# Kernel optimization log

Measured on AMD Instinct MI355X. Metric: run time of the kernel, lower is better.

The kernel has to match this reference:

```python
import jax, jax.numpy as jnp
import numpy as np

LN_EPS = 1e-5


def setup_inputs() -> dict:
    key = jax.random.key(0)
    ks = jax.random.split(key, 8)
    B, S, D = 8, 2048, 1024
    H, A, DA = 16, 4, 64
    sd = 1.0 / np.sqrt(D)
    inp = {
        "x": jax.random.normal(ks[0], (B, S, D), jnp.float32),
        "Wq": jax.random.normal(ks[1], (D, H * DA), jnp.float32) * sd,
        "bq": jnp.zeros((H * DA,), jnp.float32),
        "Wk": jax.random.normal(ks[2], (D, H * DA), jnp.float32) * sd,
        "bk": jnp.zeros((H * DA,), jnp.float32),
        "Wv": jax.random.normal(ks[3], (D, H * DA), jnp.float32) * sd,
        "bv": jnp.zeros((H * DA,), jnp.float32),
        "Wr": jax.random.normal(ks[4], (D, H), jnp.float32) * sd,
        "br": jnp.zeros((H,), jnp.float32),
        "gamma": jnp.ones((H,), jnp.float32),
        "beta": jnp.zeros((H,), jnp.float32),
        "Wo": jax.random.normal(ks[5], (A * DA, D), jnp.float32) * (1.0 / np.sqrt(A * DA)),
        "bo": jnp.zeros((D,), jnp.float32),
        "n_active": 4,
    }
    return inp


def reference(x, Wq, bq, Wk, bk, Wv, bv, Wr, br, gamma, beta, Wo, bo, n_active):
    B, S, D = x.shape
    H = Wr.shape[1]
    DA = Wq.shape[1] // H
    A = int(n_active)

    # --- router (route_type == 'mean', noise == 0) ---
    r = jnp.mean(x @ Wr + br, axis=1)                      # [B, H]
    mu = jnp.mean(r, axis=-1, keepdims=True)
    var = jnp.mean((r - mu) ** 2, axis=-1, keepdims=True)
    rn = (r - mu) * jax.lax.rsqrt(var + LN_EPS) * gamma + beta
    dist = jax.nn.softmax(rn, axis=1)                      # [B, H]

    # top-k heads; boolean-mask gather in torch selects in ascending head order
    _, idx = jax.lax.top_k(dist, A)                        # [B, A]
    idx_sorted = jnp.sort(idx, axis=-1)                    # [B, A]
    dist_dense = jnp.take_along_axis(dist, idx_sorted, axis=-1)  # [B, A]

    def proj(W, b):
        # [B, S, H*DA] -> [B, H, S, DA]
        return (x @ W + b).reshape(B, S, H, DA).transpose(0, 2, 1, 3)

    gidx = idx_sorted[:, :, None, None]                    # [B, A, 1, 1]
    Q = jnp.take_along_axis(proj(Wq, bq), gidx, axis=1)    # [B, A, S, DA]
    K = jnp.take_along_axis(proj(Wk, bk), gidx, axis=1)
    V = jnp.take_along_axis(proj(Wv, bv), gidx, axis=1)

    scale = 1.0 / jnp.sqrt(jnp.asarray(DA, x.dtype))
    scores = jnp.einsum("basd,batd->bast", Q, K) * scale   # [B, A, S, S]
    attn = jax.nn.softmax(scores, axis=-1)
    O = jnp.einsum("bast,batd->basd", attn, V)             # [B, A, S, DA]

    O = dist_dense[:, :, None, None] * O                   # gated combine
    O_final = O.transpose(0, 2, 1, 3).reshape(B, S, A * DA)
    Z = O_final @ Wo + bo                                  # [B, S, D]
    return Z
```

## Files before the change

kernel.cpp:

```cpp
#include <hip/hip_runtime.h>
#include <math.h>

#define B_ 8
#define S_ 2048
#define D_ 1024
#define H_ 16
#define A_ 4
#define DA_ 64
#define LN_EPS 1e-5f
#define QSCALE 0.1803368801111204f
#define MREF 20.0f

typedef __bf16 bf16x8 __attribute__((ext_vector_type(8)));
typedef __bf16 bf16x4 __attribute__((ext_vector_type(4)));
typedef float f32x4 __attribute__((ext_vector_type(4)));
typedef unsigned short u16x8 __attribute__((ext_vector_type(8)));
typedef unsigned short u16x4 __attribute__((ext_vector_type(4)));

static const size_t OFF_PARTIAL = 0;
static const size_t OFF_IDX     = (size_t)1 << 20;
static const size_t OFF_DIST    = ((size_t)1 << 20) + 1024;
static const size_t OFF_WOT     = ((size_t)1 << 20) + ((size_t)1 << 19);
static const size_t OFF_XB      = (size_t)2 << 20;
static const size_t OFF_OFIN    = OFF_XB;
static const size_t OFF_WT      = (size_t)34 << 20;
static const size_t OFF_Q       = (size_t)40 << 20;
static const size_t OFF_K       = (size_t)48 << 20;
static const size_t OFF_V       = (size_t)56 << 20;

__global__ __launch_bounds__(256) void k_partial(const float* __restrict__ x,
                                                 float* __restrict__ partial,
                                                 __bf16* __restrict__ xb) {
  const int c = blockIdx.x, b = blockIdx.y, t = threadIdx.x;
  const size_t base = ((size_t)b * S_ + (size_t)c * 64) * D_;
  f32x4 acc = {0.f, 0.f, 0.f, 0.f};
  for (int s = 0; s < 64; ++s) {
    f32x4 v = *(const f32x4*)(x + base + (size_t)s * D_ + 4 * t);
    acc += v;
    bf16x4 o;
    #pragma unroll
    for (int j = 0; j < 4; ++j) o[j] = (__bf16)v[j];
    *(bf16x4*)(xb + base + (size_t)s * D_ + 4 * t) = o;
  }
  *(f32x4*)(partial + ((size_t)b * 32 + c) * D_ + 4 * t) = acc;
}

__global__ __launch_bounds__(256) void k_wt(const float* __restrict__ Wq,
                                            const float* __restrict__ Wk,
                                            const float* __restrict__ Wv,
                                            __bf16* __restrict__ Wt) {
  __shared__ float tsh[64][65];
  const int n0 = blockIdx.x * 64, k0 = blockIdx.y * 64, z = blockIdx.z;
  const float* W = (z == 0) ? Wq : (z == 1) ? Wk : Wv;
  const int t = threadIdx.x;
  #pragma unroll
  for (int i = 0; i < 4; ++i) {
    int r = i * 16 + (t >> 4), c = (t & 15) * 4;
    f32x4 v = *(const f32x4*)(W + (size_t)(k0 + r) * (H_ * DA_) + n0 + c);
    tsh[r][c + 0] = v[0]; tsh[r][c + 1] = v[1]; tsh[r][c + 2] = v[2]; tsh[r][c + 3] = v[3];
  }
  __syncthreads();
  #pragma unroll
  for (int i = 0; i < 4; ++i) {
    int n = i * 16 + (t >> 4), kc = (t & 15) * 4;
    bf16x4 o;
    #pragma unroll
    for (int j = 0; j < 4; ++j) o[j] = (__bf16)tsh[kc + j][n];
    *(bf16x4*)(Wt + (size_t)z * 1048576 + (size_t)(n0 + n) * 1024 + k0 + kc) = o;
  }
}

__global__ __launch_bounds__(256) void k_wto(const float* __restrict__ Wo,
                                             __bf16* __restrict__ WoT) {
  __shared__ float tsh[64][65];
  const int n0 = blockIdx.x * 64, k0 = blockIdx.y * 64;
  const int t = threadIdx.x;
  #pragma unroll
  for (int i = 0; i < 4; ++i) {
    int r = i * 16 + (t >> 4), c = (t & 15) * 4;
    f32x4 v = *(const f32x4*)(Wo + (size_t)(k0 + r) * D_ + n0 + c);
    tsh[r][c + 0] = v[0]; tsh[r][c + 1] = v[1]; tsh[r][c + 2] = v[2]; tsh[r][c + 3] = v[3];
  }
  __syncthreads();
  #pragma unroll
  for (int i = 0; i < 4; ++i) {
    int n = i * 16 + (t >> 4), kc = (t & 15) * 4;
    bf16x4 o;
    #pragma unroll
    for (int j = 0; j < 4; ++j) o[j] = (__bf16)tsh[kc + j][n];
    *(bf16x4*)(WoT + (size_t)(n0 + n) * (A_ * DA_) + k0 + kc) = o;
  }
}

__global__ __launch_bounds__(256) void k_stats(const float* __restrict__ partial,
                                               const float* __restrict__ Wr,
                                               const float* __restrict__ br,
                                               const float* __restrict__ gamma,
                                               const float* __restrict__ beta,
                                               int* __restrict__ idx_out,
                                               float* __restrict__ dist_out) {
  __shared__ float xbar[D_];
  __shared__ float rsh[H_];
  const int b = blockIdx.x, t = threadIdx.x;
  #pragma unroll
  for (int j = 0; j < 4; ++j) {
    int d = j * 256 + t;
    float s = 0.f;
    for (int c = 0; c < 32; ++c) s += partial[((size_t)b * 32 + c) * D_ + d];
    xbar[d] = s * (1.0f / S_);
  }
  __syncthreads();
  const int w = t >> 6, lane = t & 63;
  #pragma unroll
  for (int i = 0; i < 4; ++i) {
    int h = w * 4 + i;
    float s = 0.f;
    #pragma unroll
    for (int j = 0; j < 16; ++j) {
      int d = j * 64 + lane;
      s += xbar[d] * Wr[d * H_ + h];
    }
    for (int off = 32; off; off >>= 1) s += __shfl_down(s, off);
    if (lane == 0) rsh[h] = s + br[h];
  }
  __syncthreads();
  if (t == 0) {
    float r[H_];
    float mu = 0.f;
    for (int h = 0; h < H_; ++h) { r[h] = rsh[h]; mu += r[h]; }
    mu *= (1.0f / H_);
    float var = 0.f;
    for (int h = 0; h < H_; ++h) { float d = r[h] - mu; var += d * d; }
    var *= (1.0f / H_);
    float inv = rsqrtf(var + LN_EPS);
    float rn[H_], ex[H_];
    float mx = -1e30f;
    for (int h = 0; h < H_; ++h) {
      rn[h] = (r[h] - mu) * inv * gamma[h] + beta[h];
      mx = fmaxf(mx, rn[h]);
    }
    float sum = 0.f;
    for (int h = 0; h < H_; ++h) { ex[h] = expf(rn[h] - mx); sum += ex[h]; }
    int sel[A_];
    bool used[H_] = {false};
    for (int a = 0; a < A_; ++a) {
      int best = 0; float bv = -1.f;
      for (int h = 0; h < H_; ++h)
        if (!used[h] && ex[h] > bv) { bv = ex[h]; best = h; }
      used[best] = true; sel[a] = best;
    }
    for (int i = 0; i < A_; ++i)
      for (int j = i + 1; j < A_; ++j)
        if (sel[j] < sel[i]) { int tmp = sel[i]; sel[i] = sel[j]; sel[j] = tmp; }
    float invsum = 1.0f / sum;
    for (int a = 0; a < A_; ++a) {
      idx_out[b * A_ + a] = sel[a];
      dist_out[b * A_ + a] = ex[sel[a]] * invsum;
    }
  }
}

__global__ __launch_bounds__(256) void k_qkv_mfma(const __bf16* __restrict__ xb,
                                                  const __bf16* __restrict__ Wt,
                                                  const float* __restrict__ bq,
                                                  const float* __restrict__ bk,
                                                  const float* __restrict__ bv,
                                                  const int* __restrict__ idx,
                                                  __bf16* __restrict__ Q,
                                                  __bf16* __restrict__ K,
                                                  __bf16* __restrict__ Vt_g) {
  __shared__ unsigned short As[64][72];
  __shared__ unsigned short Bs[192][72];
  const int qt = blockIdx.x, ba = blockIdx.y;
  const int b = ba >> 2;
  const int head64 = idx[ba] * 64;
  const int t = threadIdx.x;
  const int w = t >> 6, l = t & 63, x = l & 15, g = l >> 4;
  const int MO = (w >> 1) * 32, NO = (w & 1) * 96;

  const unsigned short* xbu = (const unsigned short*)xb;
  const unsigned short* Wtu = (const unsigned short*)Wt;
  const size_t xbase = ((size_t)b * S_ + (size_t)qt * 64) * D_;

  u16x8 areg[2], breg[6];
  #pragma unroll
  for (int i = 0; i < 2; ++i) {
    int id = t + 256 * i, row = id >> 3, ch = id & 7;
    areg[i] = *(const u16x8*)(xbu + xbase + (size_t)row * D_ + ch * 8);
  }
  #pragma unroll
  for (int i = 0; i < 6; ++i) {
    int id = t + 256 * i, row = id >> 3, ch = id & 7;
    int m = row >> 6, nn = row & 63;
    breg[i] = *(const u16x8*)(Wtu + (size_t)m * 1048576 +
                              (size_t)(head64 + nn) * 1024 + ch * 8);
  }

  f32x4 acc[2][6];
  #pragma unroll
  for (int mf = 0; mf < 2; ++mf)
    #pragma unroll
    for (int nf = 0; nf < 6; ++nf) acc[mf][nf] = (f32x4){0.f, 0.f, 0.f, 0.f};

  for (int k0 = 0; k0 < D_; k0 += 64) {
    __syncthreads();
    #pragma unroll
    for (int i = 0; i < 2; ++i) {
      int id = t + 256 * i, row = id >> 3, ch = id & 7;
      *(u16x8*)&As[row][ch * 8] = areg[i];
    }
    #pragma unroll
    for (int i = 0; i < 6; ++i) {
      int id = t + 256 * i, row = id >> 3, ch = id & 7;
      *(u16x8*)&Bs[row][ch * 8] = breg[i];
    }
    __syncthreads();
    {
      int kn = (k0 + 64 < D_) ? k0 + 64 : k0;
      #pragma unroll
      for (int i = 0; i < 2; ++i) {
        int id = t + 256 * i, row = id >> 3, ch = id & 7;
        areg[i] = *(const u16x8*)(xbu + xbase + (size_t)row * D_ + kn + ch * 8);
      }
      #pragma unroll
      for (int i = 0; i < 6; ++i) {
        int id = t + 256 * i, row = id >> 3, ch = id & 7;
        int m = row >> 6, nn = row & 63;
        breg[i] = *(const u16x8*)(Wtu + (size_t)m * 1048576 +
                                  (size_t)(head64 + nn) * 1024 + kn + ch * 8);
      }
    }
    #pragma unroll
    for (int ks = 0; ks < 2; ++ks) {
      bf16x8 af[2], bfr[6];
      #pragma unroll
      for (int mf = 0; mf < 2; ++mf)
        af[mf] = *(const bf16x8*)&As[MO + mf * 16 + x][ks * 32 + g * 8];
      #pragma unroll
      for (int nf = 0; nf < 6; ++nf)
        bfr[nf] = *(const bf16x8*)&Bs[NO + nf * 16 + x][ks * 32 + g * 8];
      #pragma unroll
      for (int mf = 0; mf < 2; ++mf)
        #pragma unroll
        for (int nf = 0; nf < 6; ++nf)
          acc[mf][nf] = __builtin_amdgcn_mfma_f32_16x16x32_bf16(af[mf], bfr[nf], acc[mf][nf], 0, 0, 0);
    }
  }

  #pragma unroll
  for (int nf = 0; nf < 6; ++nf) {
    const int n = NO + nf * 16;
    const int m = n >> 6;
    if (m == 2) continue;
    const float* bias = (m == 0) ? bq : bk;
    __bf16* out = (m == 0) ? Q : K;
    const float sc = (m == 0) ? QSCALE : 1.0f;
    const int nn = (n & 63) + x;
    const float bval = bias[head64 + nn];
    #pragma unroll
    for (int mf = 0; mf < 2; ++mf)
      #pragma unroll
      for (int r = 0; r < 4; ++r) {
        int srow = qt * 64 + MO + mf * 16 + 4 * g + r;
        float val = (acc[mf][nf][r] + bval) * sc;
        out[((size_t)ba * S_ + srow) * DA_ + nn] = (__bf16)val;
      }
  }

  __syncthreads();
  if (w & 1) {
    #pragma unroll
    for (int nf = 2; nf < 6; ++nf) {
      const int da = (nf - 2) * 16 + x;
      const float bval = bv[head64 + da];
      #pragma unroll
      for (int mf = 0; mf < 2; ++mf)
        #pragma unroll
        for (int r = 0; r < 4; ++r) {
          int ls = MO + mf * 16 + 4 * g + r;
          __bf16 vb = (__bf16)(acc[mf][nf][r] + bval);
          As[da][ls] = __builtin_bit_cast(unsigned short, vb);
        }
    }
  }
  __syncthreads();
  {
    unsigned short* Vtu = (unsigned short*)Vt_g;
    const int vrow = t >> 3, vch = t & 7;
    u16x8 v0 = *(const u16x8*)&As[vrow][vch * 8];
    u16x8 v1 = *(const u16x8*)&As[vrow + 32][vch * 8];
    const size_t vb0 = (size_t)ba * DA_ * S_;
    *(u16x8*)(Vtu + vb0 + (size_t)vrow * S_ + qt * 64 + vch * 8) = v0;
    *(u16x8*)(Vtu + vb0 + (size_t)(vrow + 32) * S_ + qt * 64 + vch * 8) = v1;
  }
}

__global__ __launch_bounds__(256, 4) void k_attn_mfma(const __bf16* __restrict__ Qg,
                                                      const __bf16* __restrict__ Kg,
                                                      const __bf16* __restrict__ Vtg,
                                                      const float* __restrict__ dist,
                                                      __bf16* __restrict__ Ofin) {
  __shared__ unsigned short QPs[64 * 72];
  __shared__ unsigned short Ks[64 * 64];
  __shared__ unsigned short Vt[64 * 64];

  const int qt = blockIdx.x, ba = blockIdx.y;
  const int b = ba >> 2, a = ba & 3;
  const int t = threadIdx.x;
  const int w = t >> 6, l = t & 63, x = l & 15, g = l >> 4;

  const unsigned short* Qgu = (const unsigned short*)Qg;
  const unsigned short* Kgu = (const unsigned short*)Kg;
  const unsigned short* Vgu = (const unsigned short*)Vtg;

  const size_t kvbase = (size_t)ba * S_ * DA_;
  const size_t vbase  = (size_t)ba * DA_ * S_;

  const int krow = t >> 3, kch = t & 7;

  u16x8 kreg0, kreg1, vreg0, vreg1;
  kreg0 = *(const u16x8*)(Kgu + kvbase + (size_t)(krow) * 64 + kch * 8);
  kreg1 = *(const u16x8*)(Kgu + kvbase + (size_t)(krow + 32) * 64 + kch * 8);
  vreg0 = *(const u16x8*)(Vgu + vbase + (size_t)krow * S_ + kch * 8);
  vreg1 = *(const u16x8*)(Vgu + vbase + (size_t)(krow + 32) * S_ + kch * 8);

  {
    const size_t qbase = ((size_t)ba * S_ + (size_t)qt * 64) * DA_;
    #pragma unroll
    for (int i = 0; i < 2; ++i) {
      int row = (t >> 3) + 32 * i;
      int ch = t & 7;
      u16x8 v = *(const u16x8*)(Qgu + qbase + (size_t)row * 64 + ch * 8);
      *(u16x8*)&QPs[row * 64 + ((ch ^ (row & 7)) << 3)] = v;
    }
  }
  __syncthreads();

  bf16x8 qf[2];
  #pragma unroll
  for (int ks = 0; ks < 2; ++ks) {
    int row = w * 16 + x;
    int ch = (g + 4 * ks) ^ (row & 7);
    qf[ks] = *(const bf16x8*)&QPs[row * 64 + (ch << 3)];
  }

  f32x4 o_[4];
  float l_lane = 0.f;
  #pragma unroll
  for (int nf = 0; nf < 4; ++nf) o_[nf] = (f32x4){0.f, 0.f, 0.f, 0.f};

  for (int kt = 0; kt < 32; ++kt) {
    __syncthreads();
    *(u16x8*)&Ks[krow * 64 + ((kch ^ (krow & 7)) << 3)] = kreg0;
    *(u16x8*)&Vt[krow * 64 + ((kch ^ (krow & 7)) << 3)] = vreg0;
    {
      int row1 = krow + 32;
      *(u16x8*)&Ks[row1 * 64 + ((kch ^ (row1 & 7)) << 3)] = kreg1;
      *(u16x8*)&Vt[row1 * 64 + ((kch ^ (row1 & 7)) << 3)] = vreg1;
    }
    __syncthreads();

    {
      int ktn = (kt + 1 < 32) ? kt + 1 : kt;
      kreg0 = *(const u16x8*)(Kgu + kvbase + (size_t)(ktn * 64 + krow) * 64 + kch * 8);
      kreg1 = *(const u16x8*)(Kgu + kvbase + (size_t)(ktn * 64 + krow + 32) * 64 + kch * 8);
      vreg0 = *(const u16x8*)(Vgu + vbase + (size_t)krow * S_ + ktn * 64 + kch * 8);
      vreg1 = *(const u16x8*)(Vgu + vbase + (size_t)(krow + 32) * S_ + ktn * 64 + kch * 8);
    }

    f32x4 s_[4];
    #pragma unroll
    for (int nf = 0; nf < 4; ++nf) s_[nf] = (f32x4){-MREF, -MREF, -MREF, -MREF};
    #pragma unroll
    for (int ks = 0; ks < 2; ++ks) {
      bf16x8 kf[4];
      #pragma unroll
      for (int nf = 0; nf < 4; ++nf) {
        int kvrow = nf * 16 + x;
        int ch = (g + 4 * ks) ^ (kvrow & 7);
        kf[nf] = *(const bf16x8*)&Ks[kvrow * 64 + (ch << 3)];
      }
      #pragma unroll
      for (int nf = 0; nf < 4; ++nf)
        s_[nf] = __builtin_amdgcn_mfma_f32_16x16x32_bf16(kf[nf], qf[ks], s_[nf], 0, 0, 0);
    }

    float rs = 0.f;
    #pragma unroll
    for (int nf = 0; nf < 4; ++nf)
      #pragma unroll
      for (int r = 0; r < 4; ++r) {
        float p = exp2f(s_[nf][r]);
        s_[nf][r] = p;
        rs += p;
      }
    l_lane += rs;

    #pragma unroll
    for (int nf = 0; nf < 4; ++nf) {
      u16x4 pk;
      #pragma unroll
      for (int r = 0; r < 4; ++r) {
        __bf16 pb = (__bf16)s_[nf][r];
        pk[r] = __builtin_bit_cast(unsigned short, pb);
      }
      *(u16x4*)&QPs[(w * 16 + x) * 72 + nf * 16 + 4 * g] = pk;
    }

    #pragma unroll
    for (int ks = 0; ks < 2; ++ks) {
      bf16x8 pf = *(const bf16x8*)&QPs[(w * 16 + x) * 72 + (g * 8 + ks * 32)];
      bf16x8 vf[4];
      #pragma unroll
      for (int nf = 0; nf < 4; ++nf) {
        int darow = nf * 16 + x;
        int ch = (g + 4 * ks) ^ (darow & 7);
        vf[nf] = *(const bf16x8*)&Vt[darow * 64 + (ch << 3)];
      }
      #pragma unroll
      for (int nf = 0; nf < 4; ++nf)
        o_[nf] = __builtin_amdgcn_mfma_f32_16x16x32_bf16(pf, vf[nf], o_[nf], 0, 0, 0);
    }
  }

  const float dd = dist[ba];
  {
    float lf = l_lane;
    lf += __shfl_xor(lf, 16);
    lf += __shfl_xor(lf, 32);
    float inv[4];
    #pragma unroll
    for (int r = 0; r < 4; ++r) {
      float lr = __shfl(lf, 4 * g + r);
      inv[r] = dd / lr;
    }
    #pragma unroll
    for (int nf = 0; nf < 4; ++nf)
      #pragma unroll
      for (int r = 0; r < 4; ++r) {
        int row = qt * 64 + w * 16 + 4 * g + r;
        int col = nf * 16 + x;
        Ofin[((size_t)b * S_ + row) * (A_ * DA_) + a * DA_ + col] =
            (__bf16)(o_[nf][r] * inv[r]);
      }
  }
}

__global__ __launch_bounds__(256) void k_oproj_mfma(const __bf16* __restrict__ Of,
                                                    const __bf16* __restrict__ WoT,
                                                    const float* __restrict__ bo,
                                                    float* __restrict__ Z) {
  __shared__ unsigned short As[128][72];
  __shared__ unsigned short Bs[128][72];
  const int nt = blockIdx.x, mt = blockIdx.y;
  const int t = threadIdx.x;
  const int w = t >> 6, l = t & 63, x = l & 15, g = l >> 4;
  const int MO = (w >> 1) * 64, NO = (w & 1) * 64;

  const unsigned short* Ofu = (const unsigned short*)Of;
  const unsigned short* Wu  = (const unsigned short*)WoT;

  u16x8 areg[4], breg[4];
  #pragma unroll
  for (int i = 0; i < 4; ++i) {
    int id = t + 256 * i, row = id >> 3, ch = id & 7;
    areg[i] = *(const u16x8*)(Ofu + ((size_t)(mt * 128 + row)) * (A_ * DA_) + ch * 8);
    breg[i] = *(const u16x8*)(Wu + ((size_t)(nt * 128 + row)) * (A_ * DA_) + ch * 8);
  }

  f32x4 acc[4][4];
  #pragma unroll
  for (int mf = 0; mf < 4; ++mf)
    #pragma unroll
    for (int nf = 0; nf < 4; ++nf) acc[mf][nf] = (f32x4){0.f, 0.f, 0.f, 0.f};

  for (int k0 = 0; k0 < A_ * DA_; k0 += 64) {
    __syncthreads();
    #pragma unroll
    for (int i = 0; i < 4; ++i) {
      int id = t + 256 * i, row = id >> 3, ch = id & 7;
      *(u16x8*)&As[row][ch * 8] = areg[i];
      *(u16x8*)&Bs[row][ch * 8] = breg[i];
    }
    __syncthreads();
    {
      int kn = (k0 + 64 < A_ * DA_) ? k0 + 64 : k0;
      #pragma unroll
      for (int i = 0; i < 4; ++i) {
        int id = t + 256 * i, row = id >> 3, ch = id & 7;
        areg[i] = *(const u16x8*)(Ofu + ((size_t)(mt * 128 + row)) * (A_ * DA_) + kn + ch * 8);
        breg[i] = *(const u16x8*)(Wu + ((size_t)(nt * 128 + row)) * (A_ * DA_) + kn + ch * 8);
      }
    }
    #pragma unroll
    for (int ks = 0; ks < 2; ++ks) {
      bf16x8 af[4], bfr[4];
      #pragma unroll
      for (int mf = 0; mf < 4; ++mf)
        af[mf] = *(const bf16x8*)&As[MO + mf * 16 + x][ks * 32 + g * 8];
      #pragma unroll
      for (int nf = 0; nf < 4; ++nf)
        bfr[nf] = *(const bf16x8*)&Bs[NO + nf * 16 + x][ks * 32 + g * 8];
      #pragma unroll
      for (int mf = 0; mf < 4; ++mf)
        #pragma unroll
        for (int nf = 0; nf < 4; ++nf)
          acc[mf][nf] = __builtin_amdgcn_mfma_f32_16x16x32_bf16(af[mf], bfr[nf], acc[mf][nf], 0, 0, 0);
    }
  }

  #pragma unroll
  for (int nf = 0; nf < 4; ++nf) {
    const int n = nt * 128 + NO + nf * 16 + x;
    const float bval = bo[n];
    #pragma unroll
    for (int mf = 0; mf < 4; ++mf)
      #pragma unroll
      for (int r = 0; r < 4; ++r) {
        int row = mt * 128 + MO + mf * 16 + 4 * g + r;
        Z[(size_t)row * D_ + n] = acc[mf][nf][r] + bval;
      }
  }
}

extern "C" void kernel_launch(void* const* d_in, const int* in_sizes, int n_in,
                              void* d_out, int out_size, void* d_ws, size_t ws_size,
                              hipStream_t stream) {
  const float* x     = (const float*)d_in[0];
  const float* Wq    = (const float*)d_in[1];
  const float* bq    = (const float*)d_in[2];
  const float* Wk    = (const float*)d_in[3];
  const float* bk    = (const float*)d_in[4];
  const float* Wv    = (const float*)d_in[5];
  const float* bv    = (const float*)d_in[6];
  const float* Wr    = (const float*)d_in[7];
  const float* br    = (const float*)d_in[8];
  const float* gamma = (const float*)d_in[9];
  const float* beta  = (const float*)d_in[10];
  const float* Wo    = (const float*)d_in[11];
  const float* bo    = (const float*)d_in[12];
  float* Z = (float*)d_out;

  char* ws = (char*)d_ws;
  float*  partial = (float*)(ws + OFF_PARTIAL);
  int*    idx     = (int*)(ws + OFF_IDX);
  float*  dist    = (float*)(ws + OFF_DIST);
  __bf16* WoT     = (__bf16*)(ws + OFF_WOT);
  __bf16* xb      = (__bf16*)(ws + OFF_XB);
  __bf16* Wt      = (__bf16*)(ws + OFF_WT);
  __bf16* Q       = (__bf16*)(ws + OFF_Q);
  __bf16* Ofin    = (__bf16*)(ws + OFF_OFIN);
  __bf16* K       = (__bf16*)(ws + OFF_K);
  __bf16* Vt      = (__bf16*)(ws + OFF_V);

  k_partial<<<dim3(32, B_), 256, 0, stream>>>(x, partial, xb);
  k_wt<<<dim3(16, 16, 3), 256, 0, stream>>>(Wq, Wk, Wv, Wt);
  k_wto<<<dim3(16, 4), 256, 0, stream>>>(Wo, WoT);
  k_stats<<<B_, 256, 0, stream>>>(partial, Wr, br, gamma, beta, idx, dist);
  k_qkv_mfma<<<dim3(S_ / 64, B_ * A_), 256, 0, stream>>>(xb, Wt, bq, bk, bv, idx, Q, K, Vt);
  k_attn_mfma<<<dim3(S_ / 64, B_ * A_), 256, 0, stream>>>(Q, K, Vt, dist, Ofin);
  k_oproj_mfma<<<dim3(D_ / 128, (B_ * S_) / 128), 256, 0, stream>>>(Ofin, WoT, bo, Z);
}
```

Baseline: 169.9 us.

## Switch attention kernel to 32x32x16 MFMA with KV-split across waves

Restructures the attention kernel so each wave computes a 32x32 query-by-key score tile with the 32x32x16 bf16 MFMA instead of four 16x16x32 MFMAs. The four waves are split into two query halves and two KV halves, so each wave accumulates partial outputs over half the keys. A cross-wave reduction through shared memory then merges row sums and output accumulators before the epilogue. This aims to cut LDS fragment loads per MFMA and raise MFMA efficiency, at the cost of more accumulator registers and an extra shared-memory reduction and syncs at the end.

```diff
diff --git a/kernel.cpp b/kernel.cpp
--- a/kernel.cpp
+++ b/kernel.cpp
@@ -14,6 +14,7 @@
 typedef __bf16 bf16x8 __attribute__((ext_vector_type(8)));
 typedef __bf16 bf16x4 __attribute__((ext_vector_type(4)));
 typedef float f32x4 __attribute__((ext_vector_type(4)));
+typedef float f32x16 __attribute__((ext_vector_type(16)));
 typedef unsigned short u16x8 __attribute__((ext_vector_type(8)));
 typedef unsigned short u16x4 __attribute__((ext_vector_type(4)));
 
@@ -307,7 +308,9 @@
   const int qt = blockIdx.x, ba = blockIdx.y;
   const int b = ba >> 2, a = ba & 3;
   const int t = threadIdx.x;
-  const int w = t >> 6, l = t & 63, x = l & 15, g = l >> 4;
+  const int w = t >> 6, l = t & 63;
+  const int c = l & 31, hb = l >> 5;
+  const int kvh = w & 1, qh = w >> 1;
 
   const unsigned short* Qgu = (const unsigned short*)Qg;
   const unsigned short* Kgu = (const unsigned short*)Kg;
@@ -336,18 +339,20 @@
   }
   __syncthreads();
 
-  bf16x8 qf[2];
-  #pragma unroll
-  for (int ks = 0; ks < 2; ++ks) {
-    int row = w * 16 + x;
-    int ch = (g + 4 * ks) ^ (row & 7);
-    qf[ks] = *(const bf16x8*)&QPs[row * 64 + (ch << 3)];
-  }
-
-  f32x4 o_[4];
+  bf16x8 qf[4];
+  {
+    int q = qh * 32 + c;
+    #pragma unroll
+    for (int ks = 0; ks < 4; ++ks) {
+      int ch = (ks * 2 + hb) ^ (q & 7);
+      qf[ks] = *(const bf16x8*)&QPs[q * 64 + (ch << 3)];
+    }
+  }
+
+  f32x16 o0, o1;
+  #pragma unroll
+  for (int i = 0; i < 16; ++i) { o0[i] = 0.f; o1[i] = 0.f; }
   float l_lane = 0.f;
-  #pragma unroll
-  for (int nf = 0; nf < 4; ++nf) o_[nf] = (f32x4){0.f, 0.f, 0.f, 0.f};
 
   for (int kt = 0; kt < 32; ++kt) {
     __syncthreads();
@@ -368,81 +373,95 @@
       vreg1 = *(const u16x8*)(Vgu + vbase + (size_t)(krow + 32) * S_ + ktn * 64 + kch * 8);
     }
 
-    f32x4 s_[4];
-    #pragma unroll
-    for (int nf = 0; nf < 4; ++nf) s_[nf] = (f32x4){-MREF, -MREF, -MREF, -MREF};
-    #pragma unroll
-    for (int ks = 0; ks < 2; ++ks) {
-      bf16x8 kf[4];
-      #pragma unroll
-      for (int nf = 0; nf < 4; ++nf) {
-        int kvrow = nf * 16 + x;
-        int ch = (g + 4 * ks) ^ (kvrow & 7);
-        kf[nf] = *(const bf16x8*)&Ks[kvrow * 64 + (ch << 3)];
-      }
-      #pragma unroll
-      for (int nf = 0; nf < 4; ++nf)
-        s_[nf] = __builtin_amdgcn_mfma_f32_16x16x32_bf16(kf[nf], qf[ks], s_[nf], 0, 0, 0);
+    f32x16 s;
+    #pragma unroll
+    for (int i = 0; i < 16; ++i) s[i] = -MREF;
+    #pragma unroll
+    for (int ks = 0; ks < 4; ++ks) {
+      int kv = kvh * 32 + c;
+      int ch = (ks * 2 + hb) ^ (kv & 7);
+      bf16x8 kf = *(const bf16x8*)&Ks[kv * 64 + (ch << 3)];
+      s = __builtin_amdgcn_mfma_f32_32x32x16_bf16(kf, qf[ks], s, 0, 0, 0);
     }
 
     float rs = 0.f;
     #pragma unroll
-    for (int nf = 0; nf < 4; ++nf)
-      #pragma unroll
-      for (int r = 0; r < 4; ++r) {
-        float p = exp2f(s_[nf][r]);
-        s_[nf][r] = p;
-        rs += p;
-      }
+    for (int i = 0; i < 16; ++i) {
+      float p = exp2f(s[i]);
+      s[i] = p;
+      rs += p;
+    }
     l_lane += rs;
 
     #pragma unroll
-    for (int nf = 0; nf < 4; ++nf) {
+    for (int rg = 0; rg < 4; ++rg) {
       u16x4 pk;
       #pragma unroll
-      for (int r = 0; r < 4; ++r) {
-        __bf16 pb = (__bf16)s_[nf][r];
-        pk[r] = __builtin_bit_cast(unsigned short, pb);
-      }
-      *(u16x4*)&QPs[(w * 16 + x) * 72 + nf * 16 + 4 * g] = pk;
-    }
-
-    #pragma unroll
-    for (int ks = 0; ks < 2; ++ks) {
-      bf16x8 pf = *(const bf16x8*)&QPs[(w * 16 + x) * 72 + (g * 8 + ks * 32)];
-      bf16x8 vf[4];
-      #pragma unroll
-      for (int nf = 0; nf < 4; ++nf) {
-        int darow = nf * 16 + x;
-        int ch = (g + 4 * ks) ^ (darow & 7);
-        vf[nf] = *(const bf16x8*)&Vt[darow * 64 + (ch << 3)];
-      }
-      #pragma unroll
-      for (int nf = 0; nf < 4; ++nf)
-        o_[nf] = __builtin_amdgcn_mfma_f32_16x16x32_bf16(pf, vf[nf], o_[nf], 0, 0, 0);
+      for (int rr = 0; rr < 4; ++rr) {
+        __bf16 pb = (__bf16)s[rg * 4 + rr];
+        pk[rr] = __builtin_bit_cast(unsigned short, pb);
+      }
+      int kvb = kvh * 32 + 8 * rg + 4 * hb;
+      *(u16x4*)&QPs[(qh * 32 + c) * 72 + kvb] = pk;
+    }
+
+    #pragma unroll
+    for (int ks2 = 0; ks2 < 2; ++ks2) {
+      bf16x8 pf = *(const bf16x8*)&QPs[(qh * 32 + c) * 72 + kvh * 32 + ks2 * 16 + hb * 8];
+      #pragma unroll
+      for (int dh = 0; dh < 2; ++dh) {
+        int da = dh * 32 + c;
+        int ch = (kvh * 4 + ks2 * 2 + hb) ^ (da & 7);
+        bf16x8 vf = *(const bf16x8*)&Vt[da * 64 + (ch << 3)];
+        if (dh == 0) o0 = __builtin_amdgcn_mfma_f32_32x32x16_bf16(pf, vf, o0, 0, 0, 0);
+        else         o1 = __builtin_amdgcn_mfma_f32_32x32x16_bf16(pf, vf, o1, 0, 0, 0);
+      }
     }
   }
 
   const float dd = dist[ba];
+  float* lshf = (float*)QPs;
+  float* ob0  = (float*)Ks;
+  float* ob1  = (float*)Vt;
+
+  __syncthreads();
   {
-    float lf = l_lane;
-    lf += __shfl_xor(lf, 16);
-    lf += __shfl_xor(lf, 32);
-    float inv[4];
-    #pragma unroll
-    for (int r = 0; r < 4; ++r) {
-      float lr = __shfl(lf, 4 * g + r);
-      inv[r] = dd / lr;
-    }
-    #pragma unroll
-    for (int nf = 0; nf < 4; ++nf)
-      #pragma unroll
-      for (int r = 0; r < 4; ++r) {
-        int row = qt * 64 + w * 16 + 4 * g + r;
-        int col = nf * 16 + x;
-        Ofin[((size_t)b * S_ + row) * (A_ * DA_) + a * DA_ + col] =
-            (__bf16)(o_[nf][r] * inv[r]);
-      }
+    float lf = l_lane + __shfl_xor(l_lane, 32);
+    lshf[kvh * 64 + qh * 32 + c] = lf;
+  }
+  if (kvh == 1) {
+    #pragma unroll
+    for (int i = 0; i < 16; ++i) {
+      ob0[qh * 1024 + l * 16 + i] = o0[i];
+      ob1[qh * 1024 + l * 16 + i] = o1[i];
+    }
+  }
+  __syncthreads();
+  if (t < 64) {
+    float lv = lshf[t] + lshf[64 + t];
+    lshf[128 + t] = dd / lv;
+  }
+  if (kvh == 0) {
+    #pragma unroll
+    for (int i = 0; i < 16; ++i) {
+      o0[i] += ob0[qh * 1024 + l * 16 + i];
+      o1[i] += ob1[qh * 1024 + l * 16 + i];
+    }
+  }
+  __syncthreads();
+  if (kvh == 0) {
+    #pragma unroll
+    for (int rg = 0; rg < 4; ++rg) {
+      int qloc = qh * 32 + 8 * rg + 4 * hb;
+      f32x4 linv = *(const f32x4*)&lshf[128 + qloc];
+      #pragma unroll
+      for (int rr = 0; rr < 4; ++rr) {
+        int row = qt * 64 + qloc + rr;
+        size_t obase = ((size_t)b * S_ + row) * (A_ * DA_) + a * DA_;
+        Ofin[obase + c]      = (__bf16)(o0[rg * 4 + rr] * linv[rr]);
+        Ofin[obase + 32 + c] = (__bf16)(o1[rg * 4 + rr] * linv[rr]);
+      }
+    }
   }
 }
 
```

Measured after the change: 168.7 us (median of 2 runs). About the same (-0.7%).
